# Optimization experiments

Measured on AMD Instinct MI355X. Metric: run time of the kernel, lower is better.

## Reference

```python
import jax, jax.numpy as jnp
from jax import lax
import numpy as np

NUM_STATES = 12            # 3 + num_hidden_states(9)
PERC_CH = 4 * NUM_STATES   # 48
HID = 96                   # num_hidden_features
N, H, W = 8, 512, 512


def setup_inputs() -> dict:
    key = jax.random.key(0)
    ks = jax.random.split(key, 7)
    x = jax.random.normal(ks[0], (N, NUM_STATES, H, W), dtype=jnp.float32)
    mask = jax.random.randint(ks[1], (N, NUM_STATES, H, W), 0, 2, dtype=jnp.int32)
    # perception 3x3 conv params (Conv2d default has bias)
    fan_p = NUM_STATES * 9
    pw = jax.random.uniform(ks[2], (PERC_CH, NUM_STATES, 3, 3), jnp.float32,
                            -1.0 / np.sqrt(fan_p), 1.0 / np.sqrt(fan_p))
    pb = jax.random.uniform(ks[3], (PERC_CH,), jnp.float32,
                            -1.0 / np.sqrt(fan_p), 1.0 / np.sqrt(fan_p))
    # update rule: 1x1 conv (PERC_CH->HID, bias) -> ReLU -> 1x1 conv (HID->NUM_STATES, no bias)
    w1 = jax.random.uniform(ks[4], (HID, PERC_CH), jnp.float32,
                            -1.0 / np.sqrt(PERC_CH), 1.0 / np.sqrt(PERC_CH))
    b1 = jax.random.uniform(ks[5], (HID,), jnp.float32,
                            -1.0 / np.sqrt(PERC_CH), 1.0 / np.sqrt(PERC_CH))
    w2 = jax.random.uniform(ks[6], (NUM_STATES, HID), jnp.float32,
                            -1.0 / np.sqrt(HID), 1.0 / np.sqrt(HID))
    return {"x": x, "pw": pw, "pb": pb, "w1": w1, "b1": b1, "w2": w2, "mask": mask}


def reference(x, pw, pb, w1, b1, w2, mask):
    # circular pad (matches F.pad mode='circular' with (1,1,1,1))
    y = jnp.pad(x, ((0, 0), (0, 0), (1, 1), (1, 1)), mode='wrap')
    # 3x3 VALID conv on padded input -> [N, 48, H, W]
    perc = lax.conv_general_dilated(
        y, pw, window_strides=(1, 1), padding='VALID',
        dimension_numbers=('NCHW', 'OIHW', 'NCHW')) + pb[None, :, None, None]
    # 1x1 conv -> ReLU -> 1x1 conv (per-pixel MLP)
    h = jax.nn.relu(jnp.einsum('nchw,fc->nfhw', perc, w1) + b1[None, :, None, None])
    update = jnp.einsum('nfhw,of->nohw', h, w2)
    # stochastic mask + residual
    update = update * mask.astype(x.dtype)
    return x + update
```

## Files before the change

### kernel.cpp

```cpp
#include <hip/hip_runtime.h>

typedef __attribute__((ext_vector_type(8))) short s16x8;
typedef __attribute__((ext_vector_type(4))) float f32x4;
typedef __attribute__((ext_vector_type(4))) int i32x4;

#define HW2 262144
#define NSTATE 12

__device__ __forceinline__ unsigned f2b_bits(float f) {
  unsigned u = __builtin_bit_cast(unsigned, f);
  return (u + 0x7fffu + ((u >> 16) & 1u)) >> 16;
}

__global__ void ca_prep(const float* __restrict__ pw, const float* __restrict__ pb,
                        const float* __restrict__ w1, const float* __restrict__ b1,
                        const float* __restrict__ w2,
                        short* __restrict__ A1, short* __restrict__ A2,
                        float* __restrict__ cb) {
  const int b = blockIdx.x, t = threadIdx.x;
  if (b < 30) {
    const int kf = b / 6, mf = b % 6;
    const int blk = t >> 4;
    const int row = 16 * mf + (t & 15);
    short v[8];
#pragma unroll
    for (int e = 0; e < 8; ++e) {
      const int k = 32 * kf + 8 * blk + e;
      const int sh = k >> 4, s = k & 15;
      float acc = 0.f;
      if (sh < 9 && s < 12) {
        const int ky = sh / 3, kx = sh % 3;
        for (int c = 0; c < 48; ++c)
          acc += w1[row * 48 + c] * pw[((c * 12 + s) * 3 + ky) * 3 + kx];
      }
      v[e] = (short)f2b_bits(acc);
    }
    short* dst = A1 + (b * 64 + t) * 8;
#pragma unroll
    for (int e = 0; e < 8; ++e) dst[e] = v[e];
  } else {
    const int blk = t >> 4, row = t & 15;
    for (int f = 0; f < 3; ++f) {
      short* dst = A2 + (f * 64 + t) * 8;
#pragma unroll
      for (int e = 0; e < 8; ++e) {
        const int k = 16 * (2 * f + (e >> 2)) + 4 * blk + (e & 3);
        const float val = (row < 12) ? w2[row * 96 + k] : 0.f;
        dst[e] = (short)f2b_bits(val);
      }
    }
    for (int j = t; j < 96; j += 64) {
      float a = b1[j];
      for (int c = 0; c < 48; ++c) a += w1[j * 48 + c] * pb[c];
      cb[j] = a;
    }
  }
}

#define TY 8
#define TX 64
#define LYS 10
#define LXS 66

__launch_bounds__(256, 2)
__global__ void ca_main(const float* __restrict__ x, const int* __restrict__ mask,
                        const short* __restrict__ wsA1, const short* __restrict__ wsA2,
                        const float* __restrict__ wscb, float* __restrict__ out) {
  __shared__ short lds[LYS * LXS * 16 + 8];
  const int ZOFF = LYS * LXS * 16;

  const int tid = threadIdx.x;
  const int b = blockIdx.x;
  const int n = b >> 9;
  const int rem = b & 511;
  const int y0 = (rem >> 3) * TY;
  const int x0 = (rem & 7) * TX;

  const int lane = tid & 63;
  const int blk = lane >> 4;
  const int col = lane & 15;

  s16x8 A1[5][6];
#pragma unroll
  for (int kf = 0; kf < 5; ++kf)
#pragma unroll
    for (int mf = 0; mf < 6; ++mf)
      A1[kf][mf] = *(const s16x8*)(wsA1 + ((kf * 6 + mf) * 64 + lane) * 8);
  s16x8 A2[3];
#pragma unroll
  for (int f = 0; f < 3; ++f) A2[f] = *(const s16x8*)(wsA2 + (f * 64 + lane) * 8);
  f32x4 cbv[6];
#pragma unroll
  for (int mf = 0; mf < 6; ++mf)
    cbv[mf] = *(const f32x4*)(wscb + 16 * mf + 4 * blk);

  if (tid == 0) { *(i32x4*)(lds + ZOFF) = (i32x4){0, 0, 0, 0}; }

  const int base_n = n * NSTATE;
  for (int p = tid; p < LYS * LXS; p += 256) {
    const int ly = p / LXS;
    const int lx = p - ly * LXS;
    const int gy = (y0 - 1 + ly) & 511;
    const int gx = (x0 - 1 + lx) & 511;
    const int gbase = base_n * HW2 + (gy << 9) + gx;
    unsigned bs[12];
#pragma unroll
    for (int s = 0; s < 12; ++s) bs[s] = f2b_bits(x[gbase + s * HW2]);
    i32x4 v0 = {(int)(bs[0] | (bs[1] << 16)), (int)(bs[2] | (bs[3] << 16)),
                (int)(bs[4] | (bs[5] << 16)), (int)(bs[6] | (bs[7] << 16))};
    i32x4 v1 = {(int)(bs[8] | (bs[9] << 16)), (int)(bs[10] | (bs[11] << 16)), 0, 0};
    *(i32x4*)(lds + p * 16) = v0;
    *(i32x4*)(lds + p * 16 + 8) = v1;
  }
  __syncthreads();

  const int wave = tid >> 6;
#pragma unroll 1
  for (int i = 0; i < 8; ++i) {
    const int gid = wave * 8 + i;
    const int ty = gid >> 2;
    const int tx0 = (gid & 3) << 4;

    s16x8 b1f[5];
#pragma unroll
    for (int kf = 0; kf < 5; ++kf) {
      const int sh = 2 * kf + (blk >> 1);
      const short* ap;
      if (sh < 9) {
        const int ky = sh / 3, kx = sh - 3 * (sh / 3);
        ap = lds + ((ty + ky) * LXS + (tx0 + col + kx)) * 16 + 8 * (blk & 1);
      } else {
        ap = lds + ZOFF;
      }
      b1f[kf] = *(const s16x8*)ap;
    }

    f32x4 hacc[6];
#pragma unroll
    for (int mf = 0; mf < 6; ++mf) hacc[mf] = cbv[mf];
#pragma unroll
    for (int kf = 0; kf < 5; ++kf)
#pragma unroll
      for (int mf = 0; mf < 6; ++mf)
        hacc[mf] = __builtin_amdgcn_mfma_f32_16x16x32_bf16(A1[kf][mf], b1f[kf], hacc[mf], 0, 0, 0);

    f32x4 upd = {0.f, 0.f, 0.f, 0.f};
#pragma unroll
    for (int f = 0; f < 3; ++f) {
      s16x8 b2f;
#pragma unroll
      for (int e = 0; e < 8; ++e) {
        float v = hacc[2 * f + (e >> 2)][e & 3];
        v = v > 0.f ? v : 0.f;
        b2f[e] = (short)f2b_bits(v);
      }
      upd = __builtin_amdgcn_mfma_f32_16x16x32_bf16(A2[f], b2f, upd, 0, 0, 0);
    }

    if (blk < 3) {
      const int gy = y0 + ty;
      const int gx = x0 + tx0 + col;
      const int gb = (base_n + 4 * blk) * HW2 + (gy << 9) + gx;
#pragma unroll
      for (int r = 0; r < 4; ++r) {
        const int idx = gb + r * HW2;
        out[idx] = x[idx] + upd[r] * (float)mask[idx];
      }
    }
  }
}

extern "C" void kernel_launch(void* const* d_in, const int* in_sizes, int n_in,
                              void* d_out, int out_size, void* d_ws, size_t ws_size,
                              hipStream_t stream) {
  const float* x  = (const float*)d_in[0];
  const float* pw = (const float*)d_in[1];
  const float* pb = (const float*)d_in[2];
  const float* w1 = (const float*)d_in[3];
  const float* b1 = (const float*)d_in[4];
  const float* w2 = (const float*)d_in[5];
  const int* mask = (const int*)d_in[6];
  float* out = (float*)d_out;

  short* A1 = (short*)d_ws;
  short* A2 = (short*)((char*)d_ws + 30720);
  float* cb = (float*)((char*)d_ws + 30720 + 3072);

  ca_prep<<<31, 64, 0, stream>>>(pw, pb, w1, b1, w2, A1, A2, cb);
  ca_main<<<4096, 256, 0, stream>>>(x, mask, A1, A2, cb, out);
}
```

Measured before the change: 332.9 us.

## Transpose second MFMA for vectorized epilogue and prefetch next x/mask tile

The second MFMA now takes its operands in swapped order, so each lane's accumulator holds 4 consecutive pixels of one state channel. The epilogue can then use 16-byte vector loads and stores instead of scalar strided accesses. The x and mask values for the next 16-pixel group are also loaded one iteration early, software-pipelined, to hide global latency behind the MFMA work. The cost is extra registers, and __restrict__ is dropped on wsA1 and out.

```diff
diff --git a/kernel.cpp b/kernel.cpp
--- a/kernel.cpp
+++ b/kernel.cpp
@@ -62,10 +62,13 @@
 #define LYS 10
 #define LXS 66
 
+#define EP_ADDR(gid) ((base_n + col) * HW2 + ((y0 + ((gid) >> 2)) << 9) + x0 + (((gid) & 3) << 4) + 4 * blk)
+
 __launch_bounds__(256, 2)
 __global__ void ca_main(const float* __restrict__ x, const int* __restrict__ mask,
-                        const short* __restrict__ wsA1, const short* __restrict__ wsA2,
-                        const float* __restrict__ wscb, float* __restrict__ out) {
+                        const short* wsA1,
+                        const short* __restrict__ wsA2,
+                        const float* __restrict__ wscb, float* out ) {
   __shared__ short lds[LYS * LXS * 16 + 8];
   const int ZOFF = LYS * LXS * 16;
 
@@ -115,6 +118,15 @@
   __syncthreads();
 
   const int wave = tid >> 6;
+
+  f32x4 cxq = {0.f, 0.f, 0.f, 0.f};
+  i32x4 cmq = {0, 0, 0, 0};
+  if (col < 12) {
+    const int a = EP_ADDR(wave * 8);
+    cxq = *(const f32x4*)(x + a);
+    cmq = *(const i32x4*)(mask + a);
+  }
+
 #pragma unroll 1
   for (int i = 0; i < 8; ++i) {
     const int gid = wave * 8 + i;
@@ -135,6 +147,14 @@
       b1f[kf] = *(const s16x8*)ap;
     }
 
+    f32x4 nxq = {0.f, 0.f, 0.f, 0.f};
+    i32x4 nmq = {0, 0, 0, 0};
+    if (col < 12) {
+      const int a = EP_ADDR(wave * 8 + ((i + 1) & 7));
+      nxq = *(const f32x4*)(x + a);
+      nmq = *(const i32x4*)(mask + a);
+    }
+
     f32x4 hacc[6];
 #pragma unroll
     for (int mf = 0; mf < 6; ++mf) hacc[mf] = cbv[mf];
@@ -154,19 +174,18 @@
         v = v > 0.f ? v : 0.f;
         b2f[e] = (short)f2b_bits(v);
       }
-      upd = __builtin_amdgcn_mfma_f32_16x16x32_bf16(A2[f], b2f, upd, 0, 0, 0);
-    }
-
-    if (blk < 3) {
-      const int gy = y0 + ty;
-      const int gx = x0 + tx0 + col;
-      const int gb = (base_n + 4 * blk) * HW2 + (gy << 9) + gx;
-#pragma unroll
-      for (int r = 0; r < 4; ++r) {
-        const int idx = gb + r * HW2;
-        out[idx] = x[idx] + upd[r] * (float)mask[idx];
-      }
-    }
+      upd = __builtin_amdgcn_mfma_f32_16x16x32_bf16(b2f, A2[f], upd, 0, 0, 0);
+    }
+
+    if (col < 12) {
+      const int a = EP_ADDR(gid);
+      f32x4 o;
+#pragma unroll
+      for (int r = 0; r < 4; ++r) o[r] = cxq[r] + upd[r] * (float)cmq[r];
+      *(f32x4*)(out + a) = o;
+    }
+    cxq = nxq;
+    cmq = nmq;
   }
 }
 
```

New measurement: 321.8 us. 3.4% less time.
